# Kernel optimization log

Hardware: AMD Instinct MI355X
Metric: run time of the kernel (lower is better)

The kernel has to match this reference:

```python
import jax, jax.numpy as jnp
import numpy as np

N_NODES = 100000
N_EDGES = 1600000
IN_F = 128
OUT_F = 32
NHEAD = 4
ALPHA = 0.2  # leaky relu negative slope


def setup_inputs() -> dict:
    key = jax.random.key(0)
    k1, k2, k3, k4, k5 = jax.random.split(key, 5)
    x = jax.random.normal(k1, (N_NODES, IN_F), dtype=jnp.float32)
    edge_index = jax.random.randint(k2, (2, N_EDGES), 0, N_NODES, dtype=jnp.int32)
    # glorot-ish init as in reset_parameters
    stdv_w = np.sqrt(6.0 / (IN_F + OUT_F * NHEAD))
    W = jax.random.uniform(k3, (IN_F, OUT_F * NHEAD), minval=-stdv_w, maxval=stdv_w, dtype=jnp.float32)
    stdv_a = np.sqrt(6.0 / (NHEAD + OUT_F))
    a_l = jax.random.uniform(k4, (1, NHEAD, OUT_F), minval=-stdv_a, maxval=stdv_a, dtype=jnp.float32)
    a_r = jax.random.uniform(k5, (1, NHEAD, OUT_F), minval=-stdv_a, maxval=stdv_a, dtype=jnp.float32)
    return {"x": x, "edge_index": edge_index, "W": W, "a_l": a_l, "a_r": a_r}


def reference(x, edge_index, W, a_l, a_r):
    N = x.shape[0]
    # h: [N, nhead, out]
    h = jnp.matmul(x, W).reshape(N, NHEAD, OUT_F)
    h = jnp.nan_to_num(h)
    row, col = edge_index[0], edge_index[1]
    # per-node attention halves: [N, nhead]
    al = (a_l * h).sum(axis=-1)
    ar = (a_r * h).sum(axis=-1)
    # per-edge raw scores: [E, nhead]
    e = jax.nn.leaky_relu(al[row] + ar[col], negative_slope=ALPHA)
    # segment softmax over incoming edges of each destination node (row)
    m = jax.ops.segment_max(e, row, num_segments=N)           # [N, nhead]
    e_exp = jnp.exp(e - m[row])                               # [E, nhead]
    s = jax.ops.segment_sum(e_exp, row, num_segments=N)       # [N, nhead]
    att = e_exp / s[row]                                      # [E, nhead]
    # spmm aggregation per head: out[i] = sum_{(i,j) in E} att_ij * h[j]
    msg = att[:, :, None] * h[col]                            # [E, nhead, out]
    out = jax.ops.segment_sum(msg, row, num_segments=N)       # [N, nhead, out]
    return out.reshape(N, NHEAD * OUT_F)
```

## Files before the change

### kernel.cpp

```cpp
#include <hip/hip_runtime.h>
#include <hip/hip_bf16.h>
#include <string.h>

#define NN 100000
#define NE 1600000
#define INF_ 128
#define OC 128
#define NH 4
#define ALPHA 0.2f
#define LDA 272

#define BSH 8
#define BINW 256
#define NBIN ((NN + BINW - 1) / BINW)
#define CAPB 5120
#define EPT 16
#define EPB (256 * EPT)
#define NPB1 ((NE + EPB - 1) / EPB)
#define CAP2B 6144

typedef __bf16 bf16x8 __attribute__((ext_vector_type(8)));
typedef float f32x4 __attribute__((ext_vector_type(4)));
typedef float f32x2 __attribute__((ext_vector_type(2)));

__device__ __forceinline__ float lrelu(float x) {
    return x > 0.0f ? x : ALPHA * x;
}
__device__ __forceinline__ unsigned short f2bf(float f) {
    __hip_bfloat16 b = __float2bfloat16(f);
    unsigned short u; memcpy(&u, &b, 2); return u;
}
__device__ __forceinline__ int sel4(const int4 v, int j) {
    const int lo = (j & 1) ? v.y : v.x;
    const int hi = (j & 1) ? v.w : v.z;
    return (j & 2) ? hi : lo;
}

__global__ __launch_bounds__(256) void k_pre(
    const float* __restrict__ W, const float* __restrict__ a_l,
    const float* __restrict__ a_r, __hip_bfloat16* __restrict__ Wt,
    int* __restrict__ bincur) {
    const int t = threadIdx.x;
    const int b = blockIdx.x;
    if (b < 64) {
        const int i = b * 256 + t;
        const int co = i >> 7, ko = i & 127;
        Wt[i] = __float2bfloat16(W[ko * OC + co]);
    } else {
        const int i = (b - 64) * 256 + t;
        const int cp = i >> 7, k = i & 127;
        float v = 0.f;
        if (cp < 8) {
            const int hd = cp & 3;
            const float* av = (cp < 4) ? a_l : a_r;
#pragma unroll 8
            for (int j = 0; j < 32; ++j)
                v += W[k * OC + hd * 32 + j] * av[hd * 32 + j];
        }
        Wt[(128 + cp) * 128 + k] = __float2bfloat16(v);
    }
    if (b == 0)
        for (int i = t; i < NBIN; i += 256) bincur[i] = i * CAPB;
}

__global__ __launch_bounds__(256) void k_gp1(
    const float* __restrict__ x, const __hip_bfloat16* __restrict__ Wt,
    __hip_bfloat16* __restrict__ hb, float* __restrict__ al, float* __restrict__ ar,
    const int* __restrict__ row, const int* __restrict__ col,
    int* __restrict__ bincur, unsigned* __restrict__ tmp) {
    __shared__ __align__(16) char smem[144 * LDA];
    const int tid = threadIdx.x;
    const int m5 = blockIdx.x % 5;

    if (m5 != 4) {
        char* sB = smem;
        const int gb = (blockIdx.x / 5) * 4 + m5;
        const int rowBase = gb * 64;

        for (int i4 = tid; i4 < 144 * 16; i4 += 256) {
            const int c = i4 >> 4, k4 = i4 & 15;
            *(uint4*)(sB + c * LDA + k4 * 16) =
                *(const uint4*)((const char*)Wt + (size_t)c * 256 + k4 * 16);
        }
        __syncthreads();

        const int lane = tid & 63;
        const int w = tid >> 6;
        const int arow = w * 16 + (lane & 15);
        const int grow = rowBase + arow;
        const int growc = (grow < NN) ? grow : (NN - 1);
        const int koff8 = (lane >> 4) * 8;
        const int koff = (lane >> 4) * 16;

        f32x4 acc[9];
#pragma unroll
        for (int n = 0; n < 9; ++n) acc[n] = (f32x4){0.f, 0.f, 0.f, 0.f};

#pragma unroll
        for (int kk = 0; kk < 4; ++kk) {
            const float* xp = x + (size_t)growc * INF_ + kk * 32 + koff8;
            const float4 f0 = *(const float4*)xp;
            const float4 f1 = *(const float4*)(xp + 4);
            union { bf16x8 v; unsigned short u[8]; } au;
            au.u[0] = f2bf(f0.x); au.u[1] = f2bf(f0.y);
            au.u[2] = f2bf(f0.z); au.u[3] = f2bf(f0.w);
            au.u[4] = f2bf(f1.x); au.u[5] = f2bf(f1.y);
            au.u[6] = f2bf(f1.z); au.u[7] = f2bf(f1.w);
#pragma unroll
            for (int n = 0; n < 9; ++n) {
                const int brow = n * 16 + (lane & 15);
                const bf16x8 b = *(const bf16x8*)(sB + brow * LDA + kk * 64 + koff);
                acc[n] = __builtin_amdgcn_mfma_f32_16x16x32_bf16(au.v, b, acc[n], 0, 0, 0);
            }
        }

        const int rbase = rowBase + w * 16 + (lane >> 4) * 4;
#pragma unroll
        for (int n = 0; n < 8; ++n) {
            const int cc = n * 16 + (lane & 15);
#pragma unroll
            for (int r = 0; r < 4; ++r) {
                const int rw = rbase + r;
                if (rw < NN) hb[(size_t)rw * OC + cc] = __float2bfloat16(acc[n][r]);
            }
        }
        const int cp = lane & 15;
        if (cp < 8) {
            const int hd = cp & 3;
            float* dst = (cp < 4) ? al : ar;
#pragma unroll
            for (int r = 0; r < 4; ++r) {
                const int rw = rbase + r;
                if (rw < NN) dst[rw * NH + hd] = acc[8][r];
            }
        }
    } else {
        int* h     = (int*)smem;
        int* gbase = h + NBIN;
        int* lcur  = gbase + NBIN;
        const int pb = blockIdx.x / 5;
        const int t = tid;
        for (int i = t; i < NBIN; i += 256) { h[i] = 0; lcur[i] = 0; }
        __syncthreads();

        const int e0 = pb * EPB + t * EPT;
        int r[EPT], c[EPT];
        if (e0 + EPT <= NE) {
#pragma unroll
            for (int q = 0; q < EPT / 4; ++q) {
                const int4 rv = *(const int4*)&row[e0 + q * 4];
                const int4 cv = *(const int4*)&col[e0 + q * 4];
                r[q*4+0] = rv.x; r[q*4+1] = rv.y; r[q*4+2] = rv.z; r[q*4+3] = rv.w;
                c[q*4+0] = cv.x; c[q*4+1] = cv.y; c[q*4+2] = cv.z; c[q*4+3] = cv.w;
            }
        } else {
#pragma unroll
            for (int i = 0; i < EPT; ++i) {
                const int e = e0 + i;
                r[i] = (e < NE) ? row[e] : -1;
                c[i] = (e < NE) ? col[e] : 0;
            }
        }
#pragma unroll
        for (int i = 0; i < EPT; ++i)
            if (r[i] >= 0) atomicAdd(&h[r[i] >> BSH], 1);
        __syncthreads();
        for (int i = t; i < NBIN; i += 256)
            if (h[i]) gbase[i] = atomicAdd(&bincur[i], h[i]);
        __syncthreads();
#pragma unroll
        for (int i = 0; i < EPT; ++i) {
            if (r[i] < 0) continue;
            const int b = r[i] >> BSH;
            const int pos = atomicAdd(&lcur[b], 1);
            tmp[gbase[b] + pos] =
                ((unsigned)(r[i] & (BINW - 1)) << 17) | (unsigned)c[i];
        }
    }
}

__global__ __launch_bounds__(256) void k_part2(
    const unsigned* __restrict__ tmp, const int* __restrict__ bincur,
    int2* __restrict__ nodeinfo, int* __restrict__ cols_s) {
    __shared__ unsigned stage[CAP2B];
    __shared__ int h[BINW], ts[256], cur[BINW];
    const int b = blockIdx.x, t = threadIdx.x;
    const int node0 = b * BINW;
    const int gs = b * CAPB;
    const int cnt = bincur[b] - gs;
    h[t] = 0;
    __syncthreads();
    for (int j = t; j < cnt; j += 256) {
        const unsigned p = tmp[gs + j];
        if (j < CAP2B) stage[j] = p;
        atomicAdd(&h[p >> 17], 1);
    }
    __syncthreads();
    const int v = h[t];
    ts[t] = v;
    __syncthreads();
    for (int o = 1; o < 256; o <<= 1) {
        const int add = (t >= o) ? ts[t - o] : 0;
        __syncthreads();
        ts[t] += add;
        __syncthreads();
    }
    const int ex = ts[t] - v + gs;
    cur[t] = ex;
    if (node0 + t < NN) nodeinfo[node0 + t] = make_int2(ex, v);
    __syncthreads();
    for (int j = t; j < cnt; j += 256) {
        const unsigned p = (j < CAP2B) ? stage[j] : tmp[gs + j];
        const int pos = atomicAdd(&cur[p >> 17], 1);
        cols_s[pos] = (int)(p & 0x1FFFFu);
    }
}

__global__ __launch_bounds__(256) void k_agg(
    const int2* __restrict__ nodeinfo, const int* __restrict__ cols_s,
    const float* __restrict__ al, const float* __restrict__ ar,
    const __hip_bfloat16* __restrict__ hb, float* __restrict__ out) {
    const int w = threadIdx.x >> 6;
    const int lane = threadIdx.x & 63;
    const int g = lane >> 4;
    const int sl = lane & 15;
    const int node = blockIdx.x * 16 + w * 4 + g;
    if (node >= NN) return;

    const int2 info = nodeinfo[node];
    const int start = info.x;
    const int deg = info.y;
    const int hsel = sl >> 2;
    const int je = sl >> 2;
    const int sh = sl & 3;
    const int sbase = lane & 48;
    const float al_sh = al[node * NH + sh];
    const char* hrow = (const char*)hb + sl * 16;

    f32x2 a0 = {0.f, 0.f}, a1 = {0.f, 0.f}, a2 = {0.f, 0.f}, a3 = {0.f, 0.f};
    float ssum = 0.f;

    int4 cA = *(const int4*)(cols_s + start);
    int4 cB = *(const int4*)(cols_s + start + 4);

    for (int kk = 0; kk < deg; kk += 8) {
        const int rem = deg - kk;
        const int4 cA2 = *(const int4*)(cols_s + start + kk + 8);
        const int4 cB2 = *(const int4*)(cols_s + start + kk + 12);

        float wvA = 0.f, wvB = 0.f;
        if (je < rem) {
            const int c = sel4(cA, je);
            wvA = __expf(lrelu(al_sh + ar[c * NH + sh]));
        }
        if (je + 4 < rem) {
            const int c = sel4(cB, je);
            wvB = __expf(lrelu(al_sh + ar[c * NH + sh]));
        }

        int c_[8] = {cA.x, cA.y, cA.z, cA.w, cB.x, cB.y, cB.z, cB.w};
#pragma unroll
        for (int j = 0; j < 8; ++j)
            if (j >= rem) c_[j] = 0;

#pragma unroll
        for (int j = 0; j < 8; ++j) {
            const float wj = __shfl(j < 4 ? wvA : wvB, sbase + (j & 3) * 4 + hsel);
            const uint4 v = *(const uint4*)(hrow + (size_t)c_[j] * 256);
            a0 += wj * (f32x2){__uint_as_float(v.x << 16), __uint_as_float(v.x & 0xffff0000u)};
            a1 += wj * (f32x2){__uint_as_float(v.y << 16), __uint_as_float(v.y & 0xffff0000u)};
            a2 += wj * (f32x2){__uint_as_float(v.z << 16), __uint_as_float(v.z & 0xffff0000u)};
            a3 += wj * (f32x2){__uint_as_float(v.w << 16), __uint_as_float(v.w & 0xffff0000u)};
            ssum += wj;
        }
        cA = cA2; cB = cB2;
    }

    const float inv = (ssum > 0.f) ? 1.0f / ssum : 0.f;
    float4 o0, o1;
    o0.x = a0.x * inv; o0.y = a0.y * inv; o0.z = a1.x * inv; o0.w = a1.y * inv;
    o1.x = a2.x * inv; o1.y = a2.y * inv; o1.z = a3.x * inv; o1.w = a3.y * inv;
    float* dst = out + (size_t)node * OC + sl * 8;
    *(float4*)dst = o0;
    *(float4*)(dst + 4) = o1;
}

extern "C" void kernel_launch(void* const* d_in, const int* in_sizes, int n_in,
                              void* d_out, int out_size, void* d_ws, size_t ws_size,
                              hipStream_t stream) {
    const float* x    = (const float*)d_in[0];
    const int*   ei   = (const int*)d_in[1];
    const float* W    = (const float*)d_in[2];
    const float* a_l  = (const float*)d_in[3];
    const float* a_r  = (const float*)d_in[4];
    float* out = (float*)d_out;

    const int* row = ei;
    const int* col = ei + NE;

    char* ws = (char*)d_ws;
    __hip_bfloat16* hb = (__hip_bfloat16*)ws;   ws += (size_t)NN * OC * 2;
    __hip_bfloat16* Wt = (__hip_bfloat16*)ws;   ws += (size_t)144 * 128 * 2;
    float*    al      = (float*)ws;             ws += (size_t)NN * NH * 4;
    float*    ar      = (float*)ws;             ws += (size_t)NN * NH * 4;
    int*      cols_s  = (int*)ws;               ws += (size_t)NBIN * CAPB * 4;
    unsigned* tmp     = (unsigned*)ws;          ws += (size_t)NBIN * CAPB * 4;
    int2*     nodeinfo= (int2*)ws;              ws += (size_t)NN * 8;
    int*      bincur  = (int*)ws;               ws += (size_t)NBIN * 4;

    k_pre<<<72, 256, 0, stream>>>(W, a_l, a_r, Wt, bincur);
    k_gp1<<<1955, 256, 0, stream>>>(x, Wt, hb, al, ar, row, col, bincur, tmp);
    k_part2<<<NBIN, 256, 0, stream>>>(tmp, bincur, nodeinfo, cols_s);
    k_agg<<<(NN + 15) / 16, 256, 0, stream>>>(nodeinfo, cols_s, al, ar, hb, out);
}
```

Measured before the change: 125.3 us.

## Fuse bin partition and aggregation into one kernel using shared-memory column lists

Merges the second partition pass and the aggregation kernel into a single kernel. Each block sorts its bin's edges by destination node into shared memory, with per-node lists padded to multiples of four, and then aggregates those nodes directly from shared memory. Bins shrink to 128 nodes and blocks grow to 512 threads, which removes the global cols_s and nodeinfo round-trip and one launch. In exchange there are fewer, larger blocks (about 782), more shared memory per block, and a bin capacity of 2560 edges with no overflow path.

```diff
diff --git a/kernel.cpp b/kernel.cpp
--- a/kernel.cpp
+++ b/kernel.cpp
@@ -10,14 +10,14 @@
 #define ALPHA 0.2f
 #define LDA 272
 
-#define BSH 8
-#define BINW 256
+#define BSH 7
+#define BINW 128
 #define NBIN ((NN + BINW - 1) / BINW)
-#define CAPB 5120
+#define CAPB 2560
+#define SCOLS_CAP (CAPB + 3 * BINW / 2 + 16)
 #define EPT 16
 #define EPB (256 * EPT)
 #define NPB1 ((NE + EPB - 1) / EPB)
-#define CAP2B 6144
 
 typedef __bf16 bf16x8 __attribute__((ext_vector_type(8)));
 typedef float f32x4 __attribute__((ext_vector_type(4)));
@@ -179,110 +179,112 @@
     }
 }
 
-__global__ __launch_bounds__(256) void k_part2(
+__global__ __launch_bounds__(512) void k_p2agg(
     const unsigned* __restrict__ tmp, const int* __restrict__ bincur,
-    int2* __restrict__ nodeinfo, int* __restrict__ cols_s) {
-    __shared__ unsigned stage[CAP2B];
-    __shared__ int h[BINW], ts[256], cur[BINW];
-    const int b = blockIdx.x, t = threadIdx.x;
-    const int node0 = b * BINW;
+    const float* __restrict__ al, const float* __restrict__ ar,
+    const __hip_bfloat16* __restrict__ hb, float* __restrict__ out) {
+    __shared__ __align__(16) unsigned stage[CAPB];
+    __shared__ __align__(16) int scols[SCOLS_CAP];
+    __shared__ int h[BINW], st[BINW], cur[BINW], ts[BINW];
+    const int b = blockIdx.x;
+    const int t = threadIdx.x;
     const int gs = b * CAPB;
     const int cnt = bincur[b] - gs;
-    h[t] = 0;
-    __syncthreads();
-    for (int j = t; j < cnt; j += 256) {
+
+    if (t < BINW) h[t] = 0;
+    __syncthreads();
+    for (int j = t; j < cnt; j += 512) {
         const unsigned p = tmp[gs + j];
-        if (j < CAP2B) stage[j] = p;
+        stage[j] = p;
         atomicAdd(&h[p >> 17], 1);
     }
     __syncthreads();
-    const int v = h[t];
-    ts[t] = v;
-    __syncthreads();
-    for (int o = 1; o < 256; o <<= 1) {
-        const int add = (t >= o) ? ts[t - o] : 0;
-        __syncthreads();
-        ts[t] += add;
-        __syncthreads();
-    }
-    const int ex = ts[t] - v + gs;
-    cur[t] = ex;
-    if (node0 + t < NN) nodeinfo[node0 + t] = make_int2(ex, v);
-    __syncthreads();
-    for (int j = t; j < cnt; j += 256) {
-        const unsigned p = (j < CAP2B) ? stage[j] : tmp[gs + j];
+    if (t < BINW) ts[t] = (h[t] + 3) & ~3;
+    __syncthreads();
+    for (int o = 1; o < BINW; o <<= 1) {
+        const int add = (t >= o && t < BINW) ? ts[t - o] : 0;
+        __syncthreads();
+        if (t < BINW) ts[t] += add;
+        __syncthreads();
+    }
+    if (t < BINW) {
+        const int s = ts[t] - ((h[t] + 3) & ~3);
+        st[t] = s;
+        cur[t] = s;
+    }
+    __syncthreads();
+    for (int j = t; j < cnt; j += 512) {
+        const unsigned p = stage[j];
         const int pos = atomicAdd(&cur[p >> 17], 1);
-        cols_s[pos] = (int)(p & 0x1FFFFu);
-    }
-}
-
-__global__ __launch_bounds__(256) void k_agg(
-    const int2* __restrict__ nodeinfo, const int* __restrict__ cols_s,
-    const float* __restrict__ al, const float* __restrict__ ar,
-    const __hip_bfloat16* __restrict__ hb, float* __restrict__ out) {
-    const int w = threadIdx.x >> 6;
-    const int lane = threadIdx.x & 63;
+        scols[pos] = (int)(p & 0x1FFFFu);
+    }
+    __syncthreads();
+
+    const int w = t >> 6;
+    const int lane = t & 63;
     const int g = lane >> 4;
     const int sl = lane & 15;
-    const int node = blockIdx.x * 16 + w * 4 + g;
-    if (node >= NN) return;
-
-    const int2 info = nodeinfo[node];
-    const int start = info.x;
-    const int deg = info.y;
     const int hsel = sl >> 2;
     const int je = sl >> 2;
     const int sh = sl & 3;
     const int sbase = lane & 48;
-    const float al_sh = al[node * NH + sh];
     const char* hrow = (const char*)hb + sl * 16;
 
-    f32x2 a0 = {0.f, 0.f}, a1 = {0.f, 0.f}, a2 = {0.f, 0.f}, a3 = {0.f, 0.f};
-    float ssum = 0.f;
-
-    int4 cA = *(const int4*)(cols_s + start);
-    int4 cB = *(const int4*)(cols_s + start + 4);
-
-    for (int kk = 0; kk < deg; kk += 8) {
-        const int rem = deg - kk;
-        const int4 cA2 = *(const int4*)(cols_s + start + kk + 8);
-        const int4 cB2 = *(const int4*)(cols_s + start + kk + 12);
-
-        float wvA = 0.f, wvB = 0.f;
-        if (je < rem) {
-            const int c = sel4(cA, je);
-            wvA = __expf(lrelu(al_sh + ar[c * NH + sh]));
-        }
-        if (je + 4 < rem) {
-            const int c = sel4(cB, je);
-            wvB = __expf(lrelu(al_sh + ar[c * NH + sh]));
-        }
-
-        int c_[8] = {cA.x, cA.y, cA.z, cA.w, cB.x, cB.y, cB.z, cB.w};
-#pragma unroll
-        for (int j = 0; j < 8; ++j)
-            if (j >= rem) c_[j] = 0;
-
-#pragma unroll
-        for (int j = 0; j < 8; ++j) {
-            const float wj = __shfl(j < 4 ? wvA : wvB, sbase + (j & 3) * 4 + hsel);
-            const uint4 v = *(const uint4*)(hrow + (size_t)c_[j] * 256);
-            a0 += wj * (f32x2){__uint_as_float(v.x << 16), __uint_as_float(v.x & 0xffff0000u)};
-            a1 += wj * (f32x2){__uint_as_float(v.y << 16), __uint_as_float(v.y & 0xffff0000u)};
-            a2 += wj * (f32x2){__uint_as_float(v.z << 16), __uint_as_float(v.z & 0xffff0000u)};
-            a3 += wj * (f32x2){__uint_as_float(v.w << 16), __uint_as_float(v.w & 0xffff0000u)};
-            ssum += wj;
-        }
-        cA = cA2; cB = cB2;
-    }
-
-    const float inv = (ssum > 0.f) ? 1.0f / ssum : 0.f;
-    float4 o0, o1;
-    o0.x = a0.x * inv; o0.y = a0.y * inv; o0.z = a1.x * inv; o0.w = a1.y * inv;
-    o1.x = a2.x * inv; o1.y = a2.y * inv; o1.z = a3.x * inv; o1.w = a3.y * inv;
-    float* dst = out + (size_t)node * OC + sl * 8;
-    *(float4*)dst = o0;
-    *(float4*)(dst + 4) = o1;
+    for (int rnd = 0; rnd < BINW / 32; ++rnd) {
+        const int ln = rnd * 32 + w * 4 + g;
+        const int node = b * BINW + ln;
+        if (node >= NN) continue;
+        const int start = st[ln];
+        const int deg = h[ln];
+        const float al_sh = al[node * NH + sh];
+
+        f32x2 a0 = {0.f, 0.f}, a1 = {0.f, 0.f}, a2 = {0.f, 0.f}, a3 = {0.f, 0.f};
+        float ssum = 0.f;
+
+        int4 cA = *(const int4*)(scols + start);
+        int4 cB = *(const int4*)(scols + start + 4);
+
+        for (int kk = 0; kk < deg; kk += 8) {
+            const int rem = deg - kk;
+            const int4 cA2 = *(const int4*)(scols + start + kk + 8);
+            const int4 cB2 = *(const int4*)(scols + start + kk + 12);
+
+            float wvA = 0.f, wvB = 0.f;
+            if (je < rem) {
+                const int c = sel4(cA, je);
+                wvA = __expf(lrelu(al_sh + ar[c * NH + sh]));
+            }
+            if (je + 4 < rem) {
+                const int c = sel4(cB, je);
+                wvB = __expf(lrelu(al_sh + ar[c * NH + sh]));
+            }
+
+            int c_[8] = {cA.x, cA.y, cA.z, cA.w, cB.x, cB.y, cB.z, cB.w};
+#pragma unroll
+            for (int j = 0; j < 8; ++j)
+                if (j >= rem) c_[j] = 0;
+
+#pragma unroll
+            for (int j = 0; j < 8; ++j) {
+                const float wj = __shfl(j < 4 ? wvA : wvB, sbase + (j & 3) * 4 + hsel);
+                const uint4 v = *(const uint4*)(hrow + (size_t)c_[j] * 256);
+                a0 += wj * (f32x2){__uint_as_float(v.x << 16), __uint_as_float(v.x & 0xffff0000u)};
+                a1 += wj * (f32x2){__uint_as_float(v.y << 16), __uint_as_float(v.y & 0xffff0000u)};
+                a2 += wj * (f32x2){__uint_as_float(v.z << 16), __uint_as_float(v.z & 0xffff0000u)};
+                a3 += wj * (f32x2){__uint_as_float(v.w << 16), __uint_as_float(v.w & 0xffff0000u)};
+                ssum += wj;
+            }
+            cA = cA2; cB = cB2;
+        }
+
+        const float inv = (ssum > 0.f) ? 1.0f / ssum : 0.f;
+        float4 o0, o1;
+        o0.x = a0.x * inv; o0.y = a0.y * inv; o0.z = a1.x * inv; o0.w = a1.y * inv;
+        o1.x = a2.x * inv; o1.y = a2.y * inv; o1.z = a3.x * inv; o1.w = a3.y * inv;
+        float* dst = out + (size_t)node * OC + sl * 8;
+        *(float4*)dst = o0;
+        *(float4*)(dst + 4) = o1;
+    }
 }
 
 extern "C" void kernel_launch(void* const* d_in, const int* in_sizes, int n_in,
@@ -303,13 +305,10 @@
     __hip_bfloat16* Wt = (__hip_bfloat16*)ws;   ws += (size_t)144 * 128 * 2;
     float*    al      = (float*)ws;             ws += (size_t)NN * NH * 4;
     float*    ar      = (float*)ws;             ws += (size_t)NN * NH * 4;
-    int*      cols_s  = (int*)ws;               ws += (size_t)NBIN * CAPB * 4;
     unsigned* tmp     = (unsigned*)ws;          ws += (size_t)NBIN * CAPB * 4;
-    int2*     nodeinfo= (int2*)ws;              ws += (size_t)NN * 8;
     int*      bincur  = (int*)ws;               ws += (size_t)NBIN * 4;
 
     k_pre<<<72, 256, 0, stream>>>(W, a_l, a_r, Wt, bincur);
     k_gp1<<<1955, 256, 0, stream>>>(x, Wt, hb, al, ar, row, col, bincur, tmp);
-    k_part2<<<NBIN, 256, 0, stream>>>(tmp, bincur, nodeinfo, cols_s);
-    k_agg<<<(NN + 15) / 16, 256, 0, stream>>>(nodeinfo, cols_s, al, ar, hb, out);
-}
+    k_p2agg<<<NBIN, 512, 0, stream>>>(tmp, bincur, al, ar, hb, out);
+}
```

After: 123.5 us (median of 2 runs). No clear change (-1.5%).
